# Performance work log

Hardware: AMD Instinct MI355X
Metric: run time of the kernel (lower is better)

Reference implementation:

```python
import jax, jax.numpy as jnp
import numpy as np

N = 131072
K = 1024
D = 64

def setup_inputs() -> dict:
    key = jax.random.key(0)
    k1, k2 = jax.random.split(key)
    x = jax.random.normal(k1, (N, D), dtype=jnp.float32)
    emb_weight = jax.random.normal(k2, (K, D), dtype=jnp.float32)
    return {"x": x, "emb_weight": emb_weight}

def reference(x, emb_weight):
    distances = (
        jnp.sum(x * x, axis=1, keepdims=True)
        + jnp.sum(emb_weight * emb_weight, axis=1)
        - 2.0 * jnp.matmul(x, emb_weight.T)
    )
    codebook_indices = jnp.argmin(distances, axis=1)  # [N]
    probs = jax.nn.one_hot(codebook_indices, K, dtype=x.dtype)  # [N, K]
    z_q = emb_weight[codebook_indices]  # [N, D]
    return (z_q, probs)
```

## Files before the change

### kernel.cpp

```cpp
#include <hip/hip_runtime.h>
#include <math.h>

#define N_TOK 131072
#define K_CB  1024
#define D_DIM 64
#define MARGIN_U 20u

#define WS_EN     0
#define WS_ES     4096
#define WS_CNT    266240
#define WS_LIST   266256

typedef short bf16x8 __attribute__((ext_vector_type(8)));
typedef float f32x4  __attribute__((ext_vector_type(4)));

__device__ __forceinline__ ushort f2bf(float f) {
    uint u = __float_as_uint(f);
    u += 0x7FFFu + ((u >> 16) & 1u);
    return (ushort)(u >> 16);
}
__device__ __forceinline__ float bf2f(ushort h) {
    return __uint_as_float(((uint)h) << 16);
}

__global__ __launch_bounds__(256) void prep_kernel(
    const float* __restrict__ emb, float* __restrict__ en,
    ushort* __restrict__ es, uint* __restrict__ fixcnt)
{
    const int tid = threadIdx.x;
    const int b   = blockIdx.x;
    if (b == 0 && tid == 0) *fixcnt = 0;

    const int half = tid >> 7;
    const int t    = tid & 127;
    const int cb   = b * 2 + half;
    const int jj   = t & 15;
    const int quad = (t >> 4) & 3;
    const int ks   = (t >> 6) & 1;
    const int code = cb * 16 + jj;

    const float* er = emb + (size_t)code * D_DIM + ks * 32 + quad * 8;
    f32x4 pa = *(const f32x4*)(er);
    f32x4 pb = *(const f32x4*)(er + 4);

    bf16x8 hi, lo;
    #pragma unroll
    for (int j = 0; j < 8; ++j) {
        float f = (j < 4) ? pa[j] : pb[j - 4];
        ushort h = f2bf(f);
        hi[j] = (short)h;
        lo[j] = (short)f2bf(f - bf2f(h));
    }
    bf16x8* out = (bf16x8*)es;
    out[(size_t)(cb * 4 + ks)     * 64 + quad * 16 + jj] = hi;
    out[(size_t)(cb * 4 + ks + 2) * 64 + quad * 16 + jj] = lo;

    if (tid < 32) {
        const int c2 = b * 32 + tid;
        const float* e2 = emb + (size_t)c2 * D_DIM;
        float s = 0.f;
        #pragma unroll
        for (int d = 0; d < D_DIM; ++d) s = fmaf(e2[d], e2[d], s);
        en[c2] = s;
    }
}

__global__ __launch_bounds__(256) void vq_onehot(
    const float* __restrict__ x, const float* __restrict__ emb,
    const float* __restrict__ en, const ushort* __restrict__ es,
    float* __restrict__ zq, float* __restrict__ probs,
    uint* __restrict__ fixcnt, uint* __restrict__ fixlist, uint fixcap)
{
    const int tid  = threadIdx.x;
    const int wave = tid >> 6, lane = tid & 63;
    const int quad = lane >> 4, l15 = lane & 15;
    const int rg = wave >> 1;
    const int h  = wave & 1;
    const int blockRow = blockIdx.x * 64;
    const int waveRowBase = blockRow + rg * 32;
    const bool pre = (blockIdx.x & 1) == 0;

    __shared__ uint lds_b1[2][64];
    __shared__ uint lds_b2[2][64];
    __shared__ int  lds_bk[64];

    bf16x8 af[2][4];
    #pragma unroll
    for (int g = 0; g < 2; ++g) {
        const float* xr = x + (size_t)(waveRowBase + g * 16 + l15) * D_DIM + quad * 8;
        f32x4 p0 = *(const f32x4*)(xr);
        f32x4 p1 = *(const f32x4*)(xr + 4);
        f32x4 p2 = *(const f32x4*)(xr + 32);
        f32x4 p3 = *(const f32x4*)(xr + 36);
        float v0[8], v1[8];
        #pragma unroll
        for (int j = 0; j < 4; ++j) { v0[j] = p0[j]; v0[4 + j] = p1[j]; v1[j] = p2[j]; v1[4 + j] = p3[j]; }
        #pragma unroll
        for (int j = 0; j < 8; ++j) {
            ushort h0 = f2bf(v0[j]);
            af[g][0][j] = (short)h0;
            af[g][2][j] = (short)f2bf(v0[j] - bf2f(h0));
            ushort h1 = f2bf(v1[j]);
            af[g][1][j] = (short)h1;
            af[g][3][j] = (short)f2bf(v1[j] - bf2f(h1));
        }
    }

    uint b1u[8], b2u[8];
    #pragma unroll
    for (int s = 0; s < 8; ++s) { b1u[s] = 0xFFFFFFFFu; b2u[s] = 0xFFFFFFFFu; }

    const bf16x8* __restrict__ esv = (const bf16x8*)es;
    const int fidx = quad * 16 + l15;
    const int cb0  = h * 32;

    bf16x8 bc[4]; float enc;
    #pragma unroll
    for (int ks = 0; ks < 4; ++ks) bc[ks] = esv[(size_t)cb0 * 256 + ks * 64 + fidx];
    enc = fmaf(en[cb0 * 16 + l15], 2048.f, 1048576.f);

    if (pre) {
        const f32x4 zv = {0.f, 0.f, 0.f, 0.f};
        for (int m = 0; m < 16; ++m) {
            float* prow = probs + (size_t)(blockRow + wave * 16 + m) * K_CB;
            #pragma unroll
            for (int s = 0; s < 4; ++s)
                *(f32x4*)(prow + s * 256 + lane * 4) = zv;
        }
    }

    #pragma unroll 2
    for (int i = 0; i < 32; ++i) {
        const int cb  = cb0 + i;
        const int nbi = cb0 + ((i + 1) & 31);
        bf16x8 bn[4]; float enn;
        #pragma unroll
        for (int ks = 0; ks < 4; ++ks) bn[ks] = esv[(size_t)nbi * 256 + ks * 64 + fidx];
        enn = fmaf(en[nbi * 16 + l15], 2048.f, 1048576.f);

        f32x4 acc0 = {0.f, 0.f, 0.f, 0.f};
        f32x4 acc1 = {0.f, 0.f, 0.f, 0.f};
        acc0 = __builtin_amdgcn_mfma_f32_16x16x32_bf16(af[0][0], bc[0], acc0, 0, 0, 0);
        acc0 = __builtin_amdgcn_mfma_f32_16x16x32_bf16(af[0][1], bc[1], acc0, 0, 0, 0);
        acc0 = __builtin_amdgcn_mfma_f32_16x16x32_bf16(af[0][0], bc[2], acc0, 0, 0, 0);
        acc0 = __builtin_amdgcn_mfma_f32_16x16x32_bf16(af[0][1], bc[3], acc0, 0, 0, 0);
        acc0 = __builtin_amdgcn_mfma_f32_16x16x32_bf16(af[0][2], bc[0], acc0, 0, 0, 0);
        acc0 = __builtin_amdgcn_mfma_f32_16x16x32_bf16(af[0][3], bc[1], acc0, 0, 0, 0);
        acc1 = __builtin_amdgcn_mfma_f32_16x16x32_bf16(af[1][0], bc[0], acc1, 0, 0, 0);
        acc1 = __builtin_amdgcn_mfma_f32_16x16x32_bf16(af[1][1], bc[1], acc1, 0, 0, 0);
        acc1 = __builtin_amdgcn_mfma_f32_16x16x32_bf16(af[1][0], bc[2], acc1, 0, 0, 0);
        acc1 = __builtin_amdgcn_mfma_f32_16x16x32_bf16(af[1][1], bc[3], acc1, 0, 0, 0);
        acc1 = __builtin_amdgcn_mfma_f32_16x16x32_bf16(af[1][2], bc[0], acc1, 0, 0, 0);
        acc1 = __builtin_amdgcn_mfma_f32_16x16x32_bf16(af[1][3], bc[1], acc1, 0, 0, 0);

        const uint code = (uint)(cb * 16 + l15);
        #pragma unroll
        for (int r = 0; r < 4; ++r) {
            {
                float f = fmaf(-4096.f, acc0[r], enc);
                uint u = ((uint)f << 10) | code;
                uint lo = min(b1u[r], u), hi = max(b1u[r], u);
                b1u[r] = lo; b2u[r] = min(b2u[r], hi);
            }
            {
                int s = 4 + r;
                float f = fmaf(-4096.f, acc1[r], enc);
                uint u = ((uint)f << 10) | code;
                uint lo = min(b1u[s], u), hi = max(b1u[s], u);
                b1u[s] = lo; b2u[s] = min(b2u[s], hi);
            }
        }

        #pragma unroll
        for (int ks = 0; ks < 4; ++ks) bc[ks] = bn[ks];
        enc = enn;
    }

    #pragma unroll
    for (int s = 0; s < 8; ++s) {
        #pragma unroll
        for (int off = 1; off < 16; off <<= 1) {
            uint o1 = (uint)__shfl_xor((int)b1u[s], off);
            uint o2 = (uint)__shfl_xor((int)b2u[s], off);
            uint lo = min(b1u[s], o1), hi = max(b1u[s], o1);
            b1u[s] = lo;
            b2u[s] = min(min(b2u[s], o2), hi);
        }
    }

    if (l15 == 0) {
        #pragma unroll
        for (int s = 0; s < 8; ++s) {
            int idx = rg * 32 + (s >> 2) * 16 + quad * 4 + (s & 3);
            lds_b1[h][idx] = b1u[s];
            lds_b2[h][idx] = b2u[s];
        }
    }
    __syncthreads();

    if (tid < 64) {
        uint a1 = lds_b1[0][tid], a2 = lds_b2[0][tid];
        uint c1 = lds_b1[1][tid], c2 = lds_b2[1][tid];
        uint m1 = min(a1, c1);
        uint m2 = min(min(a2, c2), max(a1, c1));
        int  mk = (int)(m1 & 1023u);
        lds_bk[tid] = mk;
        if ((m2 >> 10) - (m1 >> 10) <= MARGIN_U) {
            uint idx = atomicAdd(fixcnt, 1u);
            if (idx < fixcap) fixlist[idx] = (uint)(blockRow + tid) | ((uint)mk << 17);
        }
    }
    __syncthreads();

    #pragma unroll
    for (int mb = 0; mb < 4; ++mb) {
        int rl = wave * 16 + mb * 4 + quad;
        int bk = lds_bk[rl];
        f32x4 v = ((const f32x4*)(emb + (size_t)bk * D_DIM))[l15];
        ((f32x4*)(zq + (size_t)(blockRow + rl) * D_DIM))[l15] = v;
    }

    if (pre) {
        if (tid < 64)
            probs[(size_t)(blockRow + tid) * K_CB + lds_bk[tid]] = 1.0f;
    } else {
        for (int m = 0; m < 16; ++m) {
            int rl = wave * 16 + m;
            int bk = lds_bk[rl];
            float* prow = probs + (size_t)(blockRow + rl) * K_CB;
            #pragma unroll
            for (int s = 0; s < 4; ++s) {
                int c = s * 256 + lane * 4;
                f32x4 v;
                v[0] = (c     == bk) ? 1.f : 0.f;
                v[1] = (c + 1 == bk) ? 1.f : 0.f;
                v[2] = (c + 2 == bk) ? 1.f : 0.f;
                v[3] = (c + 3 == bk) ? 1.f : 0.f;
                *(f32x4*)(prow + c) = v;
            }
        }
    }
}

__global__ __launch_bounds__(256) void vq_fixup(
    const float* __restrict__ x, const float* __restrict__ emb,
    const float* __restrict__ en,
    float* __restrict__ zq, float* __restrict__ probs,
    const uint* __restrict__ fixcnt, const uint* __restrict__ fixlist, uint fixcap)
{
    const int lane = threadIdx.x & 63;
    const int quad = lane >> 4, l15 = lane & 15;
    const uint gwave = (uint)((blockIdx.x * 256 + threadIdx.x) >> 6);
    uint cnt = *fixcnt;
    if (cnt > fixcap) cnt = fixcap;

    for (uint e = gwave; e < cnt; e += 1024u) {
        uint w = fixlist[e];
        int row = (int)(w & 0x1FFFFu);
        int kg  = (int)(w >> 17);

        const f32x4* xr4 = (const f32x4*)(x + (size_t)row * D_DIM) + quad * 4;
        f32x4 xv[4];
        #pragma unroll
        for (int c = 0; c < 4; ++c) xv[c] = xr4[c];
        float xn = 0.f;
        #pragma unroll
        for (int c = 0; c < 4; ++c)
            #pragma unroll
            for (int j = 0; j < 4; ++j) xn = fmaf(xv[c][j], xv[c][j], xn);
        xn += __shfl_xor(xn, 16);
        xn += __shfl_xor(xn, 32);

        float bd = INFINITY; int bk = 0;
        for (int t = 0; t < 64; ++t) {
            int code = t * 16 + l15;
            const f32x4* er4 = (const f32x4*)(emb + (size_t)code * D_DIM) + quad * 4;
            float dot = 0.f;
            #pragma unroll
            for (int c = 0; c < 4; ++c) {
                f32x4 ev = er4[c];
                #pragma unroll
                for (int j = 0; j < 4; ++j) dot = fmaf(xv[c][j], ev[j], dot);
            }
            dot += __shfl_xor(dot, 16);
            dot += __shfl_xor(dot, 32);
            float dist = fmaf(-2.f, dot, xn + en[code]);
            if (dist < bd) { bd = dist; bk = code; }
        }
        #pragma unroll
        for (int off = 1; off < 16; off <<= 1) {
            float od = __shfl_xor(bd, off);
            int   ok = __shfl_xor(bk, off);
            if (od < bd || (od == bd && ok < bk)) { bd = od; bk = ok; }
        }
        if (bk != kg) {
            if (lane == 0) {
                probs[(size_t)row * K_CB + kg] = 0.f;
                probs[(size_t)row * K_CB + bk] = 1.f;
            }
            if (lane < 16)
                ((f32x4*)(zq + (size_t)row * D_DIM))[lane] =
                    ((const f32x4*)(emb + (size_t)bk * D_DIM))[lane];
        }
    }
}

extern "C" void kernel_launch(void* const* d_in, const int* in_sizes, int n_in,
                              void* d_out, int out_size, void* d_ws, size_t ws_size,
                              hipStream_t stream) {
    const float* x   = (const float*)d_in[0];
    const float* emb = (const float*)d_in[1];
    float* zq    = (float*)d_out;
    float* probs = (float*)d_out + (size_t)N_TOK * D_DIM;

    char* ws = (char*)d_ws;
    float*  en      = (float*)(ws + WS_EN);
    ushort* es      = (ushort*)(ws + WS_ES);
    uint*   fixcnt  = (uint*)(ws + WS_CNT);
    uint*   fixlist = (uint*)(ws + WS_LIST);
    uint fixcap = (ws_size > WS_LIST + 4) ? (uint)((ws_size - WS_LIST) / 4) : 0u;

    prep_kernel<<<32, 256, 0, stream>>>(emb, en, es, fixcnt);
    vq_onehot<<<N_TOK / 64, 256, 0, stream>>>(x, emb, en, es, zq, probs, fixcnt, fixlist, fixcap);
    vq_fixup<<<256, 256, 0, stream>>>(x, emb, en, zq, probs, fixcnt, fixlist, fixcap);
}
```

Measured before the change: 632.8 us.

## Split argmin and one-hot writer into separate kernels, double rows per block

The fused kernel is split in two. An argmin kernel handles 128 rows per block with 4 MFMA row groups per wave, reusing each codebook fragment across twice as many rows, and stores the chosen index in the first probs element of each row. A writer kernel then reads those indices, gathers z_q and writes the full one-hot rows. The fixup grid is doubled. The aim is to separate the compute-bound matmul/argmin from the bandwidth-bound 512MB probs write and to improve codebook reuse, at the cost of an extra launch, higher register pressure, and a round-trip of indices through global memory.

```diff
diff --git a/kernel.cpp b/kernel.cpp
--- a/kernel.cpp
+++ b/kernel.cpp
@@ -65,10 +65,10 @@
     }
 }
 
-__global__ __launch_bounds__(256) void vq_onehot(
-    const float* __restrict__ x, const float* __restrict__ emb,
+__global__ __launch_bounds__(256) void vq_argmin(
+    const float* __restrict__ x,
     const float* __restrict__ en, const ushort* __restrict__ es,
-    float* __restrict__ zq, float* __restrict__ probs,
+    float* __restrict__ probs,
     uint* __restrict__ fixcnt, uint* __restrict__ fixlist, uint fixcap)
 {
     const int tid  = threadIdx.x;
@@ -76,17 +76,15 @@
     const int quad = lane >> 4, l15 = lane & 15;
     const int rg = wave >> 1;
     const int h  = wave & 1;
-    const int blockRow = blockIdx.x * 64;
-    const int waveRowBase = blockRow + rg * 32;
-    const bool pre = (blockIdx.x & 1) == 0;
-
-    __shared__ uint lds_b1[2][64];
-    __shared__ uint lds_b2[2][64];
-    __shared__ int  lds_bk[64];
-
-    bf16x8 af[2][4];
-    #pragma unroll
-    for (int g = 0; g < 2; ++g) {
+    const int blockRow = blockIdx.x * 128;
+    const int waveRowBase = blockRow + rg * 64;
+
+    __shared__ uint lds_b1[2][128];
+    __shared__ uint lds_b2[2][128];
+
+    bf16x8 af[4][4];
+    #pragma unroll
+    for (int g = 0; g < 4; ++g) {
         const float* xr = x + (size_t)(waveRowBase + g * 16 + l15) * D_DIM + quad * 8;
         f32x4 p0 = *(const f32x4*)(xr);
         f32x4 p1 = *(const f32x4*)(xr + 4);
@@ -106,9 +104,9 @@
         }
     }
 
-    uint b1u[8], b2u[8];
-    #pragma unroll
-    for (int s = 0; s < 8; ++s) { b1u[s] = 0xFFFFFFFFu; b2u[s] = 0xFFFFFFFFu; }
+    uint b1u[16], b2u[16];
+    #pragma unroll
+    for (int s = 0; s < 16; ++s) { b1u[s] = 0xFFFFFFFFu; b2u[s] = 0xFFFFFFFFu; }
 
     const bf16x8* __restrict__ esv = (const bf16x8*)es;
     const int fidx = quad * 16 + l15;
@@ -118,16 +116,6 @@
     #pragma unroll
     for (int ks = 0; ks < 4; ++ks) bc[ks] = esv[(size_t)cb0 * 256 + ks * 64 + fidx];
     enc = fmaf(en[cb0 * 16 + l15], 2048.f, 1048576.f);
-
-    if (pre) {
-        const f32x4 zv = {0.f, 0.f, 0.f, 0.f};
-        for (int m = 0; m < 16; ++m) {
-            float* prow = probs + (size_t)(blockRow + wave * 16 + m) * K_CB;
-            #pragma unroll
-            for (int s = 0; s < 4; ++s)
-                *(f32x4*)(prow + s * 256 + lane * 4) = zv;
-        }
-    }
 
     #pragma unroll 2
     for (int i = 0; i < 32; ++i) {
@@ -138,33 +126,26 @@
         for (int ks = 0; ks < 4; ++ks) bn[ks] = esv[(size_t)nbi * 256 + ks * 64 + fidx];
         enn = fmaf(en[nbi * 16 + l15], 2048.f, 1048576.f);
 
-        f32x4 acc0 = {0.f, 0.f, 0.f, 0.f};
-        f32x4 acc1 = {0.f, 0.f, 0.f, 0.f};
-        acc0 = __builtin_amdgcn_mfma_f32_16x16x32_bf16(af[0][0], bc[0], acc0, 0, 0, 0);
-        acc0 = __builtin_amdgcn_mfma_f32_16x16x32_bf16(af[0][1], bc[1], acc0, 0, 0, 0);
-        acc0 = __builtin_amdgcn_mfma_f32_16x16x32_bf16(af[0][0], bc[2], acc0, 0, 0, 0);
-        acc0 = __builtin_amdgcn_mfma_f32_16x16x32_bf16(af[0][1], bc[3], acc0, 0, 0, 0);
-        acc0 = __builtin_amdgcn_mfma_f32_16x16x32_bf16(af[0][2], bc[0], acc0, 0, 0, 0);
-        acc0 = __builtin_amdgcn_mfma_f32_16x16x32_bf16(af[0][3], bc[1], acc0, 0, 0, 0);
-        acc1 = __builtin_amdgcn_mfma_f32_16x16x32_bf16(af[1][0], bc[0], acc1, 0, 0, 0);
-        acc1 = __builtin_amdgcn_mfma_f32_16x16x32_bf16(af[1][1], bc[1], acc1, 0, 0, 0);
-        acc1 = __builtin_amdgcn_mfma_f32_16x16x32_bf16(af[1][0], bc[2], acc1, 0, 0, 0);
-        acc1 = __builtin_amdgcn_mfma_f32_16x16x32_bf16(af[1][1], bc[3], acc1, 0, 0, 0);
-        acc1 = __builtin_amdgcn_mfma_f32_16x16x32_bf16(af[1][2], bc[0], acc1, 0, 0, 0);
-        acc1 = __builtin_amdgcn_mfma_f32_16x16x32_bf16(af[1][3], bc[1], acc1, 0, 0, 0);
+        f32x4 acc[4];
+        #pragma unroll
+        for (int g = 0; g < 4; ++g) {
+            f32x4 a = {0.f, 0.f, 0.f, 0.f};
+            a = __builtin_amdgcn_mfma_f32_16x16x32_bf16(af[g][0], bc[0], a, 0, 0, 0);
+            a = __builtin_amdgcn_mfma_f32_16x16x32_bf16(af[g][1], bc[1], a, 0, 0, 0);
+            a = __builtin_amdgcn_mfma_f32_16x16x32_bf16(af[g][0], bc[2], a, 0, 0, 0);
+            a = __builtin_amdgcn_mfma_f32_16x16x32_bf16(af[g][1], bc[3], a, 0, 0, 0);
+            a = __builtin_amdgcn_mfma_f32_16x16x32_bf16(af[g][2], bc[0], a, 0, 0, 0);
+            a = __builtin_amdgcn_mfma_f32_16x16x32_bf16(af[g][3], bc[1], a, 0, 0, 0);
+            acc[g] = a;
+        }
 
         const uint code = (uint)(cb * 16 + l15);
         #pragma unroll
-        for (int r = 0; r < 4; ++r) {
-            {
-                float f = fmaf(-4096.f, acc0[r], enc);
-                uint u = ((uint)f << 10) | code;
-                uint lo = min(b1u[r], u), hi = max(b1u[r], u);
-                b1u[r] = lo; b2u[r] = min(b2u[r], hi);
-            }
-            {
-                int s = 4 + r;
-                float f = fmaf(-4096.f, acc1[r], enc);
+        for (int g = 0; g < 4; ++g) {
+            #pragma unroll
+            for (int r = 0; r < 4; ++r) {
+                const int s = g * 4 + r;
+                float f = fmaf(-4096.f, acc[g][r], enc);
                 uint u = ((uint)f << 10) | code;
                 uint lo = min(b1u[s], u), hi = max(b1u[s], u);
                 b1u[s] = lo; b2u[s] = min(b2u[s], hi);
@@ -177,7 +158,7 @@
     }
 
     #pragma unroll
-    for (int s = 0; s < 8; ++s) {
+    for (int s = 0; s < 16; ++s) {
         #pragma unroll
         for (int off = 1; off < 16; off <<= 1) {
             uint o1 = (uint)__shfl_xor((int)b1u[s], off);
@@ -190,26 +171,40 @@
 
     if (l15 == 0) {
         #pragma unroll
-        for (int s = 0; s < 8; ++s) {
-            int idx = rg * 32 + (s >> 2) * 16 + quad * 4 + (s & 3);
+        for (int s = 0; s < 16; ++s) {
+            int idx = rg * 64 + (s >> 2) * 16 + quad * 4 + (s & 3);
             lds_b1[h][idx] = b1u[s];
             lds_b2[h][idx] = b2u[s];
         }
     }
     __syncthreads();
 
-    if (tid < 64) {
+    if (tid < 128) {
         uint a1 = lds_b1[0][tid], a2 = lds_b2[0][tid];
         uint c1 = lds_b1[1][tid], c2 = lds_b2[1][tid];
         uint m1 = min(a1, c1);
         uint m2 = min(min(a2, c2), max(a1, c1));
         int  mk = (int)(m1 & 1023u);
-        lds_bk[tid] = mk;
+        probs[(size_t)(blockRow + tid) * K_CB] = (float)mk;
         if ((m2 >> 10) - (m1 >> 10) <= MARGIN_U) {
             uint idx = atomicAdd(fixcnt, 1u);
             if (idx < fixcap) fixlist[idx] = (uint)(blockRow + tid) | ((uint)mk << 17);
         }
     }
+}
+
+__global__ __launch_bounds__(256) void vq_writer(
+    const float* __restrict__ emb,
+    float* __restrict__ zq, float* __restrict__ probs)
+{
+    const int tid  = threadIdx.x;
+    const int wave = tid >> 6, lane = tid & 63;
+    const int quad = lane >> 4, l15 = lane & 15;
+    const int blockRow = blockIdx.x * 64;
+
+    __shared__ int lds_bk[64];
+    if (tid < 64)
+        lds_bk[tid] = (int)probs[(size_t)(blockRow + tid) * K_CB];
     __syncthreads();
 
     #pragma unroll
@@ -220,24 +215,19 @@
         ((f32x4*)(zq + (size_t)(blockRow + rl) * D_DIM))[l15] = v;
     }
 
-    if (pre) {
-        if (tid < 64)
-            probs[(size_t)(blockRow + tid) * K_CB + lds_bk[tid]] = 1.0f;
-    } else {
-        for (int m = 0; m < 16; ++m) {
-            int rl = wave * 16 + m;
-            int bk = lds_bk[rl];
-            float* prow = probs + (size_t)(blockRow + rl) * K_CB;
-            #pragma unroll
-            for (int s = 0; s < 4; ++s) {
-                int c = s * 256 + lane * 4;
-                f32x4 v;
-                v[0] = (c     == bk) ? 1.f : 0.f;
-                v[1] = (c + 1 == bk) ? 1.f : 0.f;
-                v[2] = (c + 2 == bk) ? 1.f : 0.f;
-                v[3] = (c + 3 == bk) ? 1.f : 0.f;
-                *(f32x4*)(prow + c) = v;
-            }
+    for (int m = 0; m < 16; ++m) {
+        int rl = wave * 16 + m;
+        int bk = lds_bk[rl];
+        float* prow = probs + (size_t)(blockRow + rl) * K_CB;
+        #pragma unroll
+        for (int s = 0; s < 4; ++s) {
+            int c = s * 256 + lane * 4;
+            f32x4 v;
+            v[0] = (c     == bk) ? 1.f : 0.f;
+            v[1] = (c + 1 == bk) ? 1.f : 0.f;
+            v[2] = (c + 2 == bk) ? 1.f : 0.f;
+            v[3] = (c + 3 == bk) ? 1.f : 0.f;
+            *(f32x4*)(prow + c) = v;
         }
     }
 }
@@ -254,7 +244,7 @@
     uint cnt = *fixcnt;
     if (cnt > fixcap) cnt = fixcap;
 
-    for (uint e = gwave; e < cnt; e += 1024u) {
+    for (uint e = gwave; e < cnt; e += 2048u) {
         uint w = fixlist[e];
         int row = (int)(w & 0x1FFFFu);
         int kg  = (int)(w >> 17);
@@ -321,6 +311,7 @@
     uint fixcap = (ws_size > WS_LIST + 4) ? (uint)((ws_size - WS_LIST) / 4) : 0u;
 
     prep_kernel<<<32, 256, 0, stream>>>(emb, en, es, fixcnt);
-    vq_onehot<<<N_TOK / 64, 256, 0, stream>>>(x, emb, en, es, zq, probs, fixcnt, fixlist, fixcap);
-    vq_fixup<<<256, 256, 0, stream>>>(x, emb, en, zq, probs, fixcnt, fixlist, fixcap);
-}
+    vq_argmin<<<N_TOK / 128, 256, 0, stream>>>(x, en, es, probs, fixcnt, fixlist, fixcap);
+    vq_writer<<<N_TOK / 64, 256, 0, stream>>>(emb, zq, probs);
+    vq_fixup<<<512, 256, 0, stream>>>(x, emb, en, zq, probs, fixcnt, fixlist, fixcap);
+}
```

Measured after the change: 687.7 us. +8.7%, slower.

## Double-buffer codebook loads, drop pre-zeroing split, add occupancy hint

Applied to the files above, without the earlier changes.

Replaces the single-buffer prefetch loop with an explicit ping-pong of two codebook register sets (A/B) that are reloaded two iterations ahead, so global loads have more time in flight before the MFMAs need them. It also removes the split where even blocks zeroed probs before compute and wrote a single 1.0 afterwards; every block now writes the full one-hot row after compute. A launch_bounds occupancy hint of 3 is added, which may cap registers and risk spills.

```diff
diff --git a/kernel.cpp b/kernel.cpp
--- a/kernel.cpp
+++ b/kernel.cpp
@@ -21,6 +21,9 @@
 }
 __device__ __forceinline__ float bf2f(ushort h) {
     return __uint_as_float(((uint)h) << 16);
+}
+__device__ __forceinline__ f32x4 MF(bf16x8 a, bf16x8 b, f32x4 c) {
+    return __builtin_amdgcn_mfma_f32_16x16x32_bf16(a, b, c, 0, 0, 0);
 }
 
 __global__ __launch_bounds__(256) void prep_kernel(
@@ -65,7 +68,7 @@
     }
 }
 
-__global__ __launch_bounds__(256) void vq_onehot(
+__global__ __launch_bounds__(256, 3) void vq_onehot(
     const float* __restrict__ x, const float* __restrict__ emb,
     const float* __restrict__ en, const ushort* __restrict__ es,
     float* __restrict__ zq, float* __restrict__ probs,
@@ -78,7 +81,6 @@
     const int h  = wave & 1;
     const int blockRow = blockIdx.x * 64;
     const int waveRowBase = blockRow + rg * 32;
-    const bool pre = (blockIdx.x & 1) == 0;
 
     __shared__ uint lds_b1[2][64];
     __shared__ uint lds_b2[2][64];
@@ -114,67 +116,77 @@
     const int fidx = quad * 16 + l15;
     const int cb0  = h * 32;
 
-    bf16x8 bc[4]; float enc;
-    #pragma unroll
-    for (int ks = 0; ks < 4; ++ks) bc[ks] = esv[(size_t)cb0 * 256 + ks * 64 + fidx];
-    enc = fmaf(en[cb0 * 16 + l15], 2048.f, 1048576.f);
-
-    if (pre) {
-        const f32x4 zv = {0.f, 0.f, 0.f, 0.f};
-        for (int m = 0; m < 16; ++m) {
-            float* prow = probs + (size_t)(blockRow + wave * 16 + m) * K_CB;
-            #pragma unroll
-            for (int s = 0; s < 4; ++s)
-                *(f32x4*)(prow + s * 256 + lane * 4) = zv;
-        }
-    }
-
-    #pragma unroll 2
-    for (int i = 0; i < 32; ++i) {
-        const int cb  = cb0 + i;
-        const int nbi = cb0 + ((i + 1) & 31);
-        bf16x8 bn[4]; float enn;
-        #pragma unroll
-        for (int ks = 0; ks < 4; ++ks) bn[ks] = esv[(size_t)nbi * 256 + ks * 64 + fidx];
-        enn = fmaf(en[nbi * 16 + l15], 2048.f, 1048576.f);
-
-        f32x4 acc0 = {0.f, 0.f, 0.f, 0.f};
-        f32x4 acc1 = {0.f, 0.f, 0.f, 0.f};
-        acc0 = __builtin_amdgcn_mfma_f32_16x16x32_bf16(af[0][0], bc[0], acc0, 0, 0, 0);
-        acc0 = __builtin_amdgcn_mfma_f32_16x16x32_bf16(af[0][1], bc[1], acc0, 0, 0, 0);
-        acc0 = __builtin_amdgcn_mfma_f32_16x16x32_bf16(af[0][0], bc[2], acc0, 0, 0, 0);
-        acc0 = __builtin_amdgcn_mfma_f32_16x16x32_bf16(af[0][1], bc[3], acc0, 0, 0, 0);
-        acc0 = __builtin_amdgcn_mfma_f32_16x16x32_bf16(af[0][2], bc[0], acc0, 0, 0, 0);
-        acc0 = __builtin_amdgcn_mfma_f32_16x16x32_bf16(af[0][3], bc[1], acc0, 0, 0, 0);
-        acc1 = __builtin_amdgcn_mfma_f32_16x16x32_bf16(af[1][0], bc[0], acc1, 0, 0, 0);
-        acc1 = __builtin_amdgcn_mfma_f32_16x16x32_bf16(af[1][1], bc[1], acc1, 0, 0, 0);
-        acc1 = __builtin_amdgcn_mfma_f32_16x16x32_bf16(af[1][0], bc[2], acc1, 0, 0, 0);
-        acc1 = __builtin_amdgcn_mfma_f32_16x16x32_bf16(af[1][1], bc[3], acc1, 0, 0, 0);
-        acc1 = __builtin_amdgcn_mfma_f32_16x16x32_bf16(af[1][2], bc[0], acc1, 0, 0, 0);
-        acc1 = __builtin_amdgcn_mfma_f32_16x16x32_bf16(af[1][3], bc[1], acc1, 0, 0, 0);
-
-        const uint code = (uint)(cb * 16 + l15);
-        #pragma unroll
-        for (int r = 0; r < 4; ++r) {
+    bf16x8 A0, A1, A2, A3, B0, B1, B2, B3;
+    float enA, enB;
+    {
+        size_t ba = (size_t)cb0 * 256 + fidx;
+        A0 = esv[ba]; A1 = esv[ba + 64]; A2 = esv[ba + 128]; A3 = esv[ba + 192];
+        enA = fmaf(en[cb0 * 16 + l15], 2048.f, 1048576.f);
+        size_t bb = (size_t)(cb0 + 1) * 256 + fidx;
+        B0 = esv[bb]; B1 = esv[bb + 64]; B2 = esv[bb + 128]; B3 = esv[bb + 192];
+        enB = fmaf(en[(cb0 + 1) * 16 + l15], 2048.f, 1048576.f);
+    }
+
+    #define MINUPD(ACC0, ACC1, ECV, CODE) do {                                   \
+        const uint code_ = (CODE);                                               \
+        _Pragma("unroll")                                                        \
+        for (int r = 0; r < 4; ++r) {                                            \
+            {                                                                    \
+                float f_ = fmaf(-4096.f, (ACC0)[r], (ECV));                      \
+                uint u_ = ((uint)f_ << 10) | code_;                              \
+                uint lo_ = min(b1u[r], u_), hi_ = max(b1u[r], u_);               \
+                b1u[r] = lo_; b2u[r] = min(b2u[r], hi_);                         \
+            }                                                                    \
+            {                                                                    \
+                float f_ = fmaf(-4096.f, (ACC1)[r], (ECV));                      \
+                uint u_ = ((uint)f_ << 10) | code_;                              \
+                uint lo_ = min(b1u[4 + r], u_), hi_ = max(b1u[4 + r], u_);       \
+                b1u[4 + r] = lo_; b2u[4 + r] = min(b2u[4 + r], hi_);             \
+            }                                                                    \
+        }                                                                        \
+    } while (0)
+
+    for (int i = 0; i < 32; i += 2) {
+        {
+            f32x4 acc0 = {0.f, 0.f, 0.f, 0.f};
+            f32x4 acc1 = {0.f, 0.f, 0.f, 0.f};
+            acc0 = MF(af[0][0], A0, acc0); acc0 = MF(af[0][1], A1, acc0);
+            acc0 = MF(af[0][0], A2, acc0); acc0 = MF(af[0][1], A3, acc0);
+            acc0 = MF(af[0][2], A0, acc0); acc0 = MF(af[0][3], A1, acc0);
+            acc1 = MF(af[1][0], A0, acc1); acc1 = MF(af[1][1], A1, acc1);
+            acc1 = MF(af[1][0], A2, acc1); acc1 = MF(af[1][1], A3, acc1);
+            acc1 = MF(af[1][2], A0, acc1); acc1 = MF(af[1][3], A1, acc1);
+            const float ec = enA;
+            const uint  cd = (uint)((cb0 + i) * 16 + l15);
             {
-                float f = fmaf(-4096.f, acc0[r], enc);
-                uint u = ((uint)f << 10) | code;
-                uint lo = min(b1u[r], u), hi = max(b1u[r], u);
-                b1u[r] = lo; b2u[r] = min(b2u[r], hi);
+                int nc = cb0 + ((i + 2) & 31);
+                size_t bn = (size_t)nc * 256 + fidx;
+                A0 = esv[bn]; A1 = esv[bn + 64]; A2 = esv[bn + 128]; A3 = esv[bn + 192];
+                enA = fmaf(en[nc * 16 + l15], 2048.f, 1048576.f);
             }
+            MINUPD(acc0, acc1, ec, cd);
+        }
+        {
+            f32x4 acc0 = {0.f, 0.f, 0.f, 0.f};
+            f32x4 acc1 = {0.f, 0.f, 0.f, 0.f};
+            acc0 = MF(af[0][0], B0, acc0); acc0 = MF(af[0][1], B1, acc0);
+            acc0 = MF(af[0][0], B2, acc0); acc0 = MF(af[0][1], B3, acc0);
+            acc0 = MF(af[0][2], B0, acc0); acc0 = MF(af[0][3], B1, acc0);
+            acc1 = MF(af[1][0], B0, acc1); acc1 = MF(af[1][1], B1, acc1);
+            acc1 = MF(af[1][0], B2, acc1); acc1 = MF(af[1][1], B3, acc1);
+            acc1 = MF(af[1][2], B0, acc1); acc1 = MF(af[1][3], B1, acc1);
+            const float ec = enB;
+            const uint  cd = (uint)((cb0 + i + 1) * 16 + l15);
             {
-                int s = 4 + r;
-                float f = fmaf(-4096.f, acc1[r], enc);
-                uint u = ((uint)f << 10) | code;
-                uint lo = min(b1u[s], u), hi = max(b1u[s], u);
-                b1u[s] = lo; b2u[s] = min(b2u[s], hi);
+                int nc = cb0 + ((i + 3) & 31);
+                size_t bn = (size_t)nc * 256 + fidx;
+                B0 = esv[bn]; B1 = esv[bn + 64]; B2 = esv[bn + 128]; B3 = esv[bn + 192];
+                enB = fmaf(en[nc * 16 + l15], 2048.f, 1048576.f);
             }
-        }
-
-        #pragma unroll
-        for (int ks = 0; ks < 4; ++ks) bc[ks] = bn[ks];
-        enc = enn;
-    }
+            MINUPD(acc0, acc1, ec, cd);
+        }
+    }
+    #undef MINUPD
 
     #pragma unroll
     for (int s = 0; s < 8; ++s) {
@@ -220,24 +232,19 @@
         ((f32x4*)(zq + (size_t)(blockRow + rl) * D_DIM))[l15] = v;
     }
 
-    if (pre) {
-        if (tid < 64)
-            probs[(size_t)(blockRow + tid) * K_CB + lds_bk[tid]] = 1.0f;
-    } else {
-        for (int m = 0; m < 16; ++m) {
-            int rl = wave * 16 + m;
-            int bk = lds_bk[rl];
-            float* prow = probs + (size_t)(blockRow + rl) * K_CB;
-            #pragma unroll
-            for (int s = 0; s < 4; ++s) {
-                int c = s * 256 + lane * 4;
-                f32x4 v;
-                v[0] = (c     == bk) ? 1.f : 0.f;
-                v[1] = (c + 1 == bk) ? 1.f : 0.f;
-                v[2] = (c + 2 == bk) ? 1.f : 0.f;
-                v[3] = (c + 3 == bk) ? 1.f : 0.f;
-                *(f32x4*)(prow + c) = v;
-            }
+    for (int m = 0; m < 16; ++m) {
+        int rl = wave * 16 + m;
+        int bk = lds_bk[rl];
+        float* prow = probs + (size_t)(blockRow + rl) * K_CB;
+        #pragma unroll
+        for (int s = 0; s < 4; ++s) {
+            int c = s * 256 + lane * 4;
+            f32x4 v;
+            v[0] = (c     == bk) ? 1.f : 0.f;
+            v[1] = (c + 1 == bk) ? 1.f : 0.f;
+            v[2] = (c + 2 == bk) ? 1.f : 0.f;
+            v[3] = (c + 3 == bk) ? 1.f : 0.f;
+            *(f32x4*)(prow + c) = v;
         }
     }
 }
```

New measurement: 633.0 us. Within noise of the previous version (+0.0%).
